# Kernel optimization log

Measured on AMD Instinct MI355X. Metric: run time of the kernel, lower is better.

The kernel has to match this reference:

```python
import jax, jax.numpy as jnp
import numpy as np

N = 50000      # nodes
M = 600000     # message edges (rows of e2)
E = 1600000    # bond-graph edges
H = 128        # hidden_channels
OE = 256       # out_emb_channels
OC = 1         # out_channels
NL = 3         # num_output_layers
ED = 8         # edge_dim


def _glorot(key, shape):
    fan_in = shape[-1]
    return jax.random.normal(key, shape, jnp.float32) / jnp.sqrt(jnp.float32(fan_in))


def setup_inputs() -> dict:
    key = jax.random.key(0)
    ks = jax.random.split(key, 24)
    inp = {}
    inp["e2"] = jax.random.normal(ks[0], (M, H), jnp.float32)
    inp["i"] = jax.random.randint(ks[1], (M,), 0, N)
    inp["afe"] = jax.random.normal(ks[2], (N, 7), jnp.float32)
    inp["b_edge_index"] = jax.random.randint(ks[3], (2, E), 0, N)
    inp["b_edge_attr"] = jax.random.uniform(ks[4], (E, ED), jnp.float32)
    # lin_v: Linear(H+7, H)
    inp["lin_v_w"] = _glorot(ks[5], (H, H + 7))
    inp["lin_v_b"] = jnp.zeros((H,), jnp.float32)
    # PDNConv (shared across both calls): lin (no bias) + edge MLP 8->8->1
    inp["conv_lin_w"] = _glorot(ks[6], (H, H))
    inp["mlp_w1"] = _glorot(ks[7], (ED, ED))
    inp["mlp_b1"] = jnp.zeros((ED,), jnp.float32)
    inp["mlp_w2"] = _glorot(ks[8], (1, ED))
    inp["mlp_b2"] = jnp.zeros((1,), jnp.float32)
    # lin_up: Linear(H, OE)
    inp["lin_up_w"] = _glorot(ks[9], (OE, H))
    inp["lin_up_b"] = jnp.zeros((OE,), jnp.float32)
    # output MLP stack: NL x Linear(OE, OE)
    inp["lins_w"] = _glorot(ks[10], (NL, OE, OE))
    inp["lins_b"] = jnp.zeros((NL, OE), jnp.float32)
    # final lin: Linear(OE, OC, bias=False)
    inp["lin_w"] = _glorot(ks[11], (OC, OE))
    return inp


def reference(e2, i, afe, b_edge_index, b_edge_attr,
              lin_v_w, lin_v_b, conv_lin_w, mlp_w1, mlp_b1, mlp_w2, mlp_b2,
              lin_up_w, lin_up_b, lins_w, lins_b, lin_w):
    # v = scatter_sum(e2, i) over nodes
    v = jax.ops.segment_sum(e2, i, num_segments=N)          # [N, H]
    v = jnp.concatenate([v, afe], axis=1) @ lin_v_w.T + lin_v_b  # [N, H]

    # PDNConv edge weights (shared by both conv calls): mlp(edge_attr) -> sigmoid scalar
    h = jnp.maximum(b_edge_attr @ mlp_w1.T + mlp_b1, 0.0)
    ew = jax.nn.sigmoid(h @ mlp_w2.T + mlp_b2)[:, 0]        # [E]
    row, col = b_edge_index[0], b_edge_index[1]
    # gcn_norm (no self loops): deg over destination, symmetric normalization
    deg = jax.ops.segment_sum(ew, col, num_segments=N)
    dinv = jnp.where(deg > 0, jax.lax.rsqrt(jnp.maximum(deg, 1e-30)), 0.0)
    norm = dinv[row] * ew * dinv[col]                        # [E]

    def conv(x):
        xw = x @ conv_lin_w.T                                # [N, H]
        return jax.ops.segment_sum(xw[row] * norm[:, None], col, num_segments=N)

    v = conv(v)
    v = conv(v)
    v = jax.nn.relu(v)

    v = v @ lin_up_w.T + lin_up_b                            # [N, OE]
    for l in range(NL):
        v = jax.nn.relu(v @ lins_w[l].T + lins_b[l])
    v = v @ lin_w.T                                          # [N, OC]
    return v
```

## Files before the change

### kernel.cpp

```cpp
#include <hip/hip_runtime.h>


#define Nn 50000
#define Mm 600000
#define Ee 1600000
#define NB 196

typedef unsigned short u16;
typedef unsigned int u32;
typedef __attribute__((ext_vector_type(8))) short bh8;
typedef __attribute__((ext_vector_type(4))) float f4;

__device__ __forceinline__ float bf2f(u16 u) {
    union { u32 i; float f; } v; v.i = ((u32)u) << 16; return v.f;
}
__device__ __forceinline__ u16 f2bf(float f) {
    union { float f; u32 u; } v; v.f = f;
    return (u16)((v.u + 0x7fffu + ((v.u >> 16) & 1u)) >> 16);
}

__global__ __launch_bounds__(256) void k_edge(
    const float* __restrict__ attr, const int* __restrict__ eidx,
    const float* __restrict__ w1, const float* __restrict__ b1,
    const float* __restrict__ w2, const float* __restrict__ b2,
    float* __restrict__ ew, float* __restrict__ deg, int* __restrict__ cntC)
{
    __shared__ float sW1[64], sB1[8], sW2[8], sB2;
    int t = threadIdx.x;
    if (t < 64) sW1[t] = w1[t];
    if (t < 8) { sB1[t] = b1[t]; sW2[t] = w2[t]; }
    if (t == 0) sB2 = b2[0];
    __syncthreads();
    int e = blockIdx.x * 256 + t;
    if (e >= Ee) return;
    float4 q0 = *(const float4*)(attr + (size_t)e * 8);
    float4 q1 = *(const float4*)(attr + (size_t)e * 8 + 4);
    float a[8] = { q0.x, q0.y, q0.z, q0.w, q1.x, q1.y, q1.z, q1.w };
    float z = sB2;
#pragma unroll
    for (int j = 0; j < 8; ++j) {
        float h = sB1[j];
#pragma unroll
        for (int k = 0; k < 8; ++k) h += a[k] * sW1[j * 8 + k];
        z += fmaxf(h, 0.f) * sW2[j];
    }
    float s = 1.f / (1.f + __expf(-z));
    ew[e] = s;
    int c = eidx[Ee + e];
    atomicAdd(&deg[c], s);
    atomicAdd(&cntC[c], 1);
}

__global__ __launch_bounds__(256) void k_cntm(const int* __restrict__ ii,
                                              int* __restrict__ cnt)
{
    int m = blockIdx.x * 256 + threadIdx.x;
    if (m < Mm) atomicAdd(&cnt[ii[m]], 1);
}

__global__ __launch_bounds__(256) void k_scanA(
    const int* __restrict__ cnt, int* __restrict__ loc, int* __restrict__ part)
{
    __shared__ int buf[256];
    int t = threadIdx.x, i = blockIdx.x * 256 + t;
    int v = (i < Nn) ? cnt[i] : 0;
    buf[t] = v;
    __syncthreads();
#pragma unroll
    for (int d = 1; d < 256; d <<= 1) {
        int x = (t >= d) ? buf[t - d] : 0;
        __syncthreads();
        buf[t] += x;
        __syncthreads();
    }
    if (i < Nn) loc[i] = buf[t] - v;
    if (t == 255) part[blockIdx.x] = buf[255];
}

__global__ __launch_bounds__(256) void k_scanB(int* __restrict__ pA,
                                               int* __restrict__ pB)
{
    int* p = blockIdx.x ? pB : pA;
    __shared__ int buf[256];
    int t = threadIdx.x;
    int v = (t < NB) ? p[t] : 0;
    buf[t] = v;
    __syncthreads();
#pragma unroll
    for (int d = 1; d < 256; d <<= 1) {
        int x = (t >= d) ? buf[t - d] : 0;
        __syncthreads();
        buf[t] += x;
        __syncthreads();
    }
    if (t < NB) p[t] = buf[t] - v;
}

__global__ __launch_bounds__(256) void k_scanC(
    const int* __restrict__ cnt, const int* __restrict__ part,
    int* __restrict__ off, int* __restrict__ cur,
    const float* __restrict__ deg, float* __restrict__ dinv)
{
    int t = threadIdx.x, i = blockIdx.x * 256 + t;
    if (i >= Nn) return;
    int v = off[i] + part[blockIdx.x];
    off[i] = v;
    cur[i] = v;
    if (i == Nn - 1) off[Nn] = v + cnt[i];
    if (dinv) {
        float d = deg[i];
        dinv[i] = (d > 0.f) ? rsqrtf(fmaxf(d, 1e-30f)) : 0.f;
    }
}

__global__ __launch_bounds__(256) void k_scatter_col(
    const int* __restrict__ eidx, const float* __restrict__ ew,
    const float* __restrict__ dinv, int* __restrict__ cur,
    int2* __restrict__ edgep)
{
    int e = blockIdx.x * 256 + threadIdx.x;
    if (e >= Ee) return;
    int r = eidx[e], c = eidx[Ee + e];
    float nm = dinv[r] * ew[e] * dinv[c];
    int idx = atomicAdd(&cur[c], 1);
    edgep[idx] = make_int2(r, __float_as_int(nm));
}

__global__ __launch_bounds__(256) void k_scatter_m(
    const int* __restrict__ ii, int* __restrict__ cur, int* __restrict__ midx)
{
    int m = blockIdx.x * 256 + threadIdx.x;
    if (m >= Mm) return;
    midx[atomicAdd(&cur[ii[m]], 1)] = m;
}

__global__ __launch_bounds__(256) void k_segsum(
    const int* __restrict__ offM, const int* __restrict__ midx,
    const float* __restrict__ e2, const float* __restrict__ afe,
    float* __restrict__ Xcat)
{
    int wv = threadIdx.x >> 6, lane = threadIdx.x & 63;
    int n = blockIdx.x * 4 + wv;
    if (n >= Nn) return;
    int j0 = offM[n], j1 = offM[n + 1];
    float a0 = 0.f, a1 = 0.f;
    int j = j0;
    if (j < j1) {
        int m = midx[j];
        float2 p = *(const float2*)(e2 + (size_t)m * 128 + lane * 2);
        for (++j; j < j1; ++j) {
            int m2 = midx[j];
            float2 p2 = *(const float2*)(e2 + (size_t)m2 * 128 + lane * 2);
            a0 += p.x; a1 += p.y;
            p = p2;
        }
        a0 += p.x; a1 += p.y;
    }
    *(float2*)(Xcat + (size_t)n * 160 + lane * 2) = make_float2(a0, a1);
    if (lane < 32) {
        int ch = 128 + lane;
        float v = (ch < 135) ? afe[(size_t)n * 7 + (ch - 128)] : 0.f;
        Xcat[(size_t)n * 160 + ch] = v;
    }
}

__global__ __launch_bounds__(256) void k_splitw(
    const float* __restrict__ src, u16* __restrict__ h, u16* __restrict__ l,
    int rows, int sc, int dc)
{
    int idx = blockIdx.x * 256 + threadIdx.x;
    if (idx >= rows * dc) return;
    int r = idx / dc, c = idx % dc;
    float x = (c < sc) ? src[(size_t)r * sc + c] : 0.f;
    u16 hh = f2bf(x);
    h[idx] = hh;
    l[idx] = f2bf(x - bf2f(hh));
}

__global__ __launch_bounds__(256) void k_gemm(
    const float* __restrict__ X, const u16* __restrict__ Wh,
    const u16* __restrict__ Wl, const float* __restrict__ bias,
    void* __restrict__ Y, int M, int K, int NO, int flags)
{
    __shared__ __align__(16) u16 Ah[128][40];
    __shared__ __align__(16) u16 Al[128][40];
    __shared__ __align__(16) u16 Bh[128][40];
    __shared__ __align__(16) u16 Bl[128][40];
    const int t = threadIdx.x;
    const int m0 = blockIdx.x * 128, n0 = blockIdx.y * 128;
    const int lane = t & 63, wv = t >> 6;
    const int wm = (wv >> 1) * 64, wn = (wv & 1) * 64;
    const int lr = lane & 15, lq = lane >> 4;
    const int srow = t >> 1, skc = (t & 1) * 16;
    const bool aok = (m0 + srow) < M;
    const float* Xp = X + (size_t)(m0 + srow) * K + skc;
    const u16* Whp = Wh + (size_t)(n0 + srow) * K + skc;
    const u16* Wlp = Wl + (size_t)(n0 + srow) * K + skc;
    f4 acc[4][4] = {};

    for (int k0 = 0; k0 < K; k0 += 32) {
        float av[16];
#pragma unroll
        for (int g = 0; g < 4; ++g) {
            float4 v = make_float4(0.f, 0.f, 0.f, 0.f);
            if (aok) v = *(const float4*)(Xp + k0 + g * 4);
            av[g * 4 + 0] = v.x; av[g * 4 + 1] = v.y;
            av[g * 4 + 2] = v.z; av[g * 4 + 3] = v.w;
        }
        uint4 bh0 = *(const uint4*)(Whp + k0);
        uint4 bh1 = *(const uint4*)(Whp + k0 + 8);
        uint4 bl0 = *(const uint4*)(Wlp + k0);
        uint4 bl1 = *(const uint4*)(Wlp + k0 + 8);
        __syncthreads();
#pragma unroll
        for (int g = 0; g < 4; ++g) {
            union { u16 s[4]; uint2 d; } h, l;
#pragma unroll
            for (int j = 0; j < 4; ++j) {
                float x = av[g * 4 + j];
                u16 hh = f2bf(x);
                h.s[j] = hh; l.s[j] = f2bf(x - bf2f(hh));
            }
            *(uint2*)&Ah[srow][skc + g * 4] = h.d;
            *(uint2*)&Al[srow][skc + g * 4] = l.d;
        }
        *(uint4*)&Bh[srow][skc]     = bh0;
        *(uint4*)&Bh[srow][skc + 8] = bh1;
        *(uint4*)&Bl[srow][skc]     = bl0;
        *(uint4*)&Bl[srow][skc + 8] = bl1;
        __syncthreads();
        bh8 fah[4], fal[4], fbh[4], fbl[4];
#pragma unroll
        for (int i = 0; i < 4; ++i) {
            fah[i] = *(const bh8*)&Ah[wm + i * 16 + lr][lq * 8];
            fal[i] = *(const bh8*)&Al[wm + i * 16 + lr][lq * 8];
            fbh[i] = *(const bh8*)&Bh[wn + i * 16 + lr][lq * 8];
            fbl[i] = *(const bh8*)&Bl[wn + i * 16 + lr][lq * 8];
        }
#pragma unroll
        for (int mi = 0; mi < 4; ++mi)
#pragma unroll
            for (int ni = 0; ni < 4; ++ni) {
                acc[mi][ni] = __builtin_amdgcn_mfma_f32_16x16x32_bf16(
                    fah[mi], fbh[ni], acc[mi][ni], 0, 0, 0);
                acc[mi][ni] = __builtin_amdgcn_mfma_f32_16x16x32_bf16(
                    fal[mi], fbh[ni], acc[mi][ni], 0, 0, 0);
                acc[mi][ni] = __builtin_amdgcn_mfma_f32_16x16x32_bf16(
                    fah[mi], fbl[ni], acc[mi][ni], 0, 0, 0);
            }
    }
#pragma unroll
    for (int ni = 0; ni < 4; ++ni) {
        int gn = n0 + wn + ni * 16 + lr;
        float bv = bias ? bias[gn] : 0.f;
#pragma unroll
        for (int mi = 0; mi < 4; ++mi) {
#pragma unroll
            for (int r = 0; r < 4; ++r) {
                int gm = m0 + wm + mi * 16 + lq * 4 + r;
                if (gm < M) {
                    float v = acc[mi][ni][r] + bv;
                    if (flags & 1) v = fmaxf(v, 0.f);
                    if (flags & 2) ((u16*)Y)[(size_t)gm * NO + gn] = f2bf(v);
                    else           ((float*)Y)[(size_t)gm * NO + gn] = v;
                }
            }
        }
    }
}

__global__ __launch_bounds__(256) void k_gather(
    const int* __restrict__ off, const int2* __restrict__ edgep,
    const u16* __restrict__ xw, float* __restrict__ out, int relu)
{
    int wv = threadIdx.x >> 6, lane = threadIdx.x & 63;
    int n = blockIdx.x * 4 + wv;
    if (n >= Nn) return;
    int j0 = off[n], j1 = off[n + 1];
    float a0 = 0.f, a1 = 0.f;
    int j = j0;
    if (j < j1) {
        int2 ep = edgep[j];
        u32 p = *(const u32*)(xw + (size_t)ep.x * 128 + lane * 2);
        for (++j; j < j1; ++j) {
            int2 ep2 = edgep[j];
            u32 p2 = *(const u32*)(xw + (size_t)ep2.x * 128 + lane * 2);
            float w = __int_as_float(ep.y);
            a0 += w * bf2f((u16)(p & 0xffff));
            a1 += w * bf2f((u16)(p >> 16));
            ep = ep2; p = p2;
        }
        float w = __int_as_float(ep.y);
        a0 += w * bf2f((u16)(p & 0xffff));
        a1 += w * bf2f((u16)(p >> 16));
    }
    if (relu) { a0 = fmaxf(a0, 0.f); a1 = fmaxf(a1, 0.f); }
    *(float2*)(out + (size_t)n * 128 + lane * 2) = make_float2(a0, a1);
}

__global__ __launch_bounds__(256) void k_final(
    const float* __restrict__ S, const float* __restrict__ lw,
    float* __restrict__ out)
{
    __shared__ float w[256];
    int t = threadIdx.x;
    w[t] = lw[t];
    __syncthreads();
    int n = blockIdx.x * 4 + (t >> 6);
    int lane = t & 63;
    if (n >= Nn) return;
    float s = 0.f;
#pragma unroll
    for (int k = 0; k < 4; ++k)
        s += S[(size_t)n * 256 + lane + k * 64] * w[lane + k * 64];
#pragma unroll
    for (int d = 32; d >= 1; d >>= 1) s += __shfl_xor(s, d, 64);
    if (lane == 0) out[n] = s;
}

extern "C" void kernel_launch(void* const* d_in, const int* in_sizes, int n_in,
                              void* d_out, int out_size, void* d_ws, size_t ws_size,
                              hipStream_t stream)
{
    (void)in_sizes; (void)n_in; (void)out_size; (void)ws_size;
    const float* e2       = (const float*)d_in[0];
    const int*   iidx     = (const int*)d_in[1];
    const float* afe      = (const float*)d_in[2];
    const int*   bei      = (const int*)d_in[3];
    const float* battr    = (const float*)d_in[4];
    const float* lin_v_w  = (const float*)d_in[5];
    const float* lin_v_b  = (const float*)d_in[6];
    const float* conv_w   = (const float*)d_in[7];
    const float* w1       = (const float*)d_in[8];
    const float* b1       = (const float*)d_in[9];
    const float* w2       = (const float*)d_in[10];
    const float* b2       = (const float*)d_in[11];
    const float* lin_up_w = (const float*)d_in[12];
    const float* lin_up_b = (const float*)d_in[13];
    const float* lins_w   = (const float*)d_in[14];
    const float* lins_b   = (const float*)d_in[15];
    const float* lin_w    = (const float*)d_in[16];

    char* ws = (char*)d_ws;
    int2*  edgep = (int2*) (ws + 0);
    float* Xcat  = (float*)(ws + 12800000);
    float* s0    = (float*)(ws + 12800000);
    float* v1    = (float*)(ws + 64000000);
    u16*   xw    = (u16*)  (ws + 89600000);
    float* s1    = (float*)(ws + 64000000);
    float* ew    = (float*)(ws + 102400000);
    int*   midx  = (int*)  (ws + 108800000);
    int*   cntC  = (int*)  (ws + 115200000);
    int*   cntM  = (int*)  (ws + 115400000);
    float* deg   = (float*)(ws + 115600000);
    int*   offC  = (int*)  (ws + 115800000);
    int*   curC  = (int*)  (ws + 116000256);
    int*   offM  = (int*)  (ws + 116200256);
    int*   curM  = (int*)  (ws + 116400512);
    float* dinv  = (float*)(ws + 116600512);
    u16*   Wh    = (u16*)  (ws + 116800512);
    u16*   Wl    = (u16*)  (ws + 117332992);
    int*   partC = (int*)  (ws + 117865472);
    int*   partM = (int*)  (ws + 117866368);

    const int oWv = 0, oConv = 20480, oLup = 36864, oLins = 69632;

    hipMemsetAsync(ws + 115200000, 0, 3 * Nn * 4, stream);

    k_edge<<<(Ee + 255) / 256, 256, 0, stream>>>(battr, bei, w1, b1, w2, b2,
                                                 ew, deg, cntC);
    k_cntm<<<(Mm + 255) / 256, 256, 0, stream>>>(iidx, cntM);
    k_scanA<<<NB, 256, 0, stream>>>(cntC, offC, partC);
    k_scanA<<<NB, 256, 0, stream>>>(cntM, offM, partM);
    k_scanB<<<2, 256, 0, stream>>>(partC, partM);
    k_scanC<<<NB, 256, 0, stream>>>(cntC, partC, offC, curC, deg, dinv);
    k_scanC<<<NB, 256, 0, stream>>>(cntM, partM, offM, curM, nullptr, nullptr);
    k_scatter_col<<<(Ee + 255) / 256, 256, 0, stream>>>(bei, ew, dinv, curC,
                                                        edgep);
    k_scatter_m<<<(Mm + 255) / 256, 256, 0, stream>>>(iidx, curM, midx);
    k_segsum<<<(Nn + 3) / 4, 256, 0, stream>>>(offM, midx, e2, afe, Xcat);

    k_splitw<<<(128 * 160 + 255) / 256, 256, 0, stream>>>(
        lin_v_w, Wh + oWv, Wl + oWv, 128, 135, 160);
    k_splitw<<<(128 * 128 + 255) / 256, 256, 0, stream>>>(
        conv_w, Wh + oConv, Wl + oConv, 128, 128, 128);
    k_splitw<<<(256 * 128 + 255) / 256, 256, 0, stream>>>(
        lin_up_w, Wh + oLup, Wl + oLup, 256, 128, 128);
    k_splitw<<<(768 * 256 + 255) / 256, 256, 0, stream>>>(
        lins_w, Wh + oLins, Wl + oLins, 768, 256, 256);

#define GEMM(Xp, WO, Bp, Yp, M_, K_, NO_, FL_)                                \
    k_gemm<<<dim3(((M_) + 127) / 128, (NO_) / 128), 256, 0, stream>>>(        \
        (const float*)(Xp), Wh + (WO), Wl + (WO), (const float*)(Bp),         \
        (void*)(Yp), M_, K_, NO_, FL_)

    GEMM(Xcat, oWv, lin_v_b, v1, Nn, 160, 128, 0);
    GEMM(v1, oConv, nullptr, xw, Nn, 128, 128, 2);
    k_gather<<<(Nn + 3) / 4, 256, 0, stream>>>(offC, edgep, xw, v1, 0);
    GEMM(v1, oConv, nullptr, xw, Nn, 128, 128, 2);
    k_gather<<<(Nn + 3) / 4, 256, 0, stream>>>(offC, edgep, xw, v1, 1);
    GEMM(v1, oLup, lin_up_b, s0, Nn, 128, 256, 0);
    GEMM(s0, oLins + 0 * 65536, lins_b + 0,   s1, Nn, 256, 256, 1);
    GEMM(s1, oLins + 1 * 65536, lins_b + 256, s0, Nn, 256, 256, 1);
    GEMM(s0, oLins + 2 * 65536, lins_b + 512, s1, Nn, 256, 256, 1);
    k_final<<<(Nn + 3) / 4, 256, 0, stream>>>(s1, lin_w, (float*)d_out);
#undef GEMM
}
```

Measured before the change: 1.235 ms.

## Store activations pre-split as bf16 hi/lo planes and stage GEMM tiles via global_load_lds

Producer kernels (segsum, gather, GEMM epilogue) now write activations as separate bf16 high and low planes instead of fp32. The GEMM no longer converts fp32 to split bf16 on every tile load. Each of the four waves stages one plane directly into LDS with 16-byte global_load_lds, and out-of-range rows are clamped. This removes the per-tile conversion ALU work and register staging. The trade-offs are an unpadded LDS layout that may cause bank conflicts, no prefetch overlap since each load is followed by a barrier, and a larger workspace footprint.

```diff
diff --git a/kernel.cpp b/kernel.cpp
--- a/kernel.cpp
+++ b/kernel.cpp
@@ -18,6 +18,11 @@
     union { float f; u32 u; } v; v.f = f;
     return (u16)((v.u + 0x7fffu + ((v.u >> 16) & 1u)) >> 16);
 }
+
+#define GLD16(gp, lp)                                                         \
+    __builtin_amdgcn_global_load_lds(                                         \
+        (const __attribute__((address_space(1))) unsigned int*)(gp),          \
+        (__attribute__((address_space(3))) unsigned int*)(lp), 16, 0, 0)
 
 __global__ __launch_bounds__(256) void k_edge(
     const float* __restrict__ attr, const int* __restrict__ eidx,
@@ -137,7 +142,7 @@
 __global__ __launch_bounds__(256) void k_segsum(
     const int* __restrict__ offM, const int* __restrict__ midx,
     const float* __restrict__ e2, const float* __restrict__ afe,
-    float* __restrict__ Xcat)
+    u16* __restrict__ XH, u16* __restrict__ XL)
 {
     int wv = threadIdx.x >> 6, lane = threadIdx.x & 63;
     int n = blockIdx.x * 4 + wv;
@@ -156,11 +161,16 @@
         }
         a0 += p.x; a1 += p.y;
     }
-    *(float2*)(Xcat + (size_t)n * 160 + lane * 2) = make_float2(a0, a1);
+    u16 h0 = f2bf(a0), h1 = f2bf(a1);
+    u16 l0 = f2bf(a0 - bf2f(h0)), l1 = f2bf(a1 - bf2f(h1));
+    *(u32*)&XH[(size_t)n * 160 + lane * 2] = (u32)h0 | ((u32)h1 << 16);
+    *(u32*)&XL[(size_t)n * 160 + lane * 2] = (u32)l0 | ((u32)l1 << 16);
     if (lane < 32) {
         int ch = 128 + lane;
         float v = (ch < 135) ? afe[(size_t)n * 7 + (ch - 128)] : 0.f;
-        Xcat[(size_t)n * 160 + ch] = v;
+        u16 h = f2bf(v);
+        XH[(size_t)n * 160 + ch] = h;
+        XL[(size_t)n * 160 + ch] = f2bf(v - bf2f(h));
     }
 }
 
@@ -178,64 +188,42 @@
 }
 
 __global__ __launch_bounds__(256) void k_gemm(
-    const float* __restrict__ X, const u16* __restrict__ Wh,
-    const u16* __restrict__ Wl, const float* __restrict__ bias,
-    void* __restrict__ Y, int M, int K, int NO, int flags)
-{
-    __shared__ __align__(16) u16 Ah[128][40];
-    __shared__ __align__(16) u16 Al[128][40];
-    __shared__ __align__(16) u16 Bh[128][40];
-    __shared__ __align__(16) u16 Bl[128][40];
+    const u16* __restrict__ Ah, const u16* __restrict__ Al,
+    const u16* __restrict__ Bh, const u16* __restrict__ Bl,
+    const float* __restrict__ bias, u16* __restrict__ Yh, u16* __restrict__ Yl,
+    int M, int K, int NO, int flags)
+{
+    __shared__ __align__(16) u16 sT[4][128 * 32];
     const int t = threadIdx.x;
     const int m0 = blockIdx.x * 128, n0 = blockIdx.y * 128;
     const int lane = t & 63, wv = t >> 6;
     const int wm = (wv >> 1) * 64, wn = (wv & 1) * 64;
     const int lr = lane & 15, lq = lane >> 4;
-    const int srow = t >> 1, skc = (t & 1) * 16;
-    const bool aok = (m0 + srow) < M;
-    const float* Xp = X + (size_t)(m0 + srow) * K + skc;
-    const u16* Whp = Wh + (size_t)(n0 + srow) * K + skc;
-    const u16* Wlp = Wl + (size_t)(n0 + srow) * K + skc;
+    const u16* gplane = (wv == 0) ? Ah : (wv == 1) ? Al : (wv == 2) ? Bh : Bl;
+    u16* lplane = &sT[wv][0];
+    const int rbase = (wv < 2) ? m0 : n0;
+    const int rlim = (wv < 2) ? (M - 1) : 0x7fffffff;
+    const int srow = lane >> 2;
+    const int scol = (lane & 3) * 8;
     f4 acc[4][4] = {};
 
     for (int k0 = 0; k0 < K; k0 += 32) {
-        float av[16];
-#pragma unroll
-        for (int g = 0; g < 4; ++g) {
-            float4 v = make_float4(0.f, 0.f, 0.f, 0.f);
-            if (aok) v = *(const float4*)(Xp + k0 + g * 4);
-            av[g * 4 + 0] = v.x; av[g * 4 + 1] = v.y;
-            av[g * 4 + 2] = v.z; av[g * 4 + 3] = v.w;
+        __syncthreads();
+#pragma unroll
+        for (int i = 0; i < 8; ++i) {
+            int grow = rbase + i * 16 + srow;
+            if (grow > rlim) grow = rlim;
+            const u16* gp = gplane + (size_t)grow * K + k0 + scol;
+            GLD16(gp, lplane + i * 512);
         }
-        uint4 bh0 = *(const uint4*)(Whp + k0);
-        uint4 bh1 = *(const uint4*)(Whp + k0 + 8);
-        uint4 bl0 = *(const uint4*)(Wlp + k0);
-        uint4 bl1 = *(const uint4*)(Wlp + k0 + 8);
-        __syncthreads();
-#pragma unroll
-        for (int g = 0; g < 4; ++g) {
-            union { u16 s[4]; uint2 d; } h, l;
-#pragma unroll
-            for (int j = 0; j < 4; ++j) {
-                float x = av[g * 4 + j];
-                u16 hh = f2bf(x);
-                h.s[j] = hh; l.s[j] = f2bf(x - bf2f(hh));
-            }
-            *(uint2*)&Ah[srow][skc + g * 4] = h.d;
-            *(uint2*)&Al[srow][skc + g * 4] = l.d;
-        }
-        *(uint4*)&Bh[srow][skc]     = bh0;
-        *(uint4*)&Bh[srow][skc + 8] = bh1;
-        *(uint4*)&Bl[srow][skc]     = bl0;
-        *(uint4*)&Bl[srow][skc + 8] = bl1;
         __syncthreads();
         bh8 fah[4], fal[4], fbh[4], fbl[4];
 #pragma unroll
         for (int i = 0; i < 4; ++i) {
-            fah[i] = *(const bh8*)&Ah[wm + i * 16 + lr][lq * 8];
-            fal[i] = *(const bh8*)&Al[wm + i * 16 + lr][lq * 8];
-            fbh[i] = *(const bh8*)&Bh[wn + i * 16 + lr][lq * 8];
-            fbl[i] = *(const bh8*)&Bl[wn + i * 16 + lr][lq * 8];
+            fah[i] = *(const bh8*)&sT[0][(wm + i * 16 + lr) * 32 + lq * 8];
+            fal[i] = *(const bh8*)&sT[1][(wm + i * 16 + lr) * 32 + lq * 8];
+            fbh[i] = *(const bh8*)&sT[2][(wn + i * 16 + lr) * 32 + lq * 8];
+            fbl[i] = *(const bh8*)&sT[3][(wn + i * 16 + lr) * 32 + lq * 8];
         }
 #pragma unroll
         for (int mi = 0; mi < 4; ++mi)
@@ -261,8 +249,10 @@
                 if (gm < M) {
                     float v = acc[mi][ni][r] + bv;
                     if (flags & 1) v = fmaxf(v, 0.f);
-                    if (flags & 2) ((u16*)Y)[(size_t)gm * NO + gn] = f2bf(v);
-                    else           ((float*)Y)[(size_t)gm * NO + gn] = v;
+                    u16 h = f2bf(v);
+                    Yh[(size_t)gm * NO + gn] = h;
+                    if (!(flags & 2))
+                        Yl[(size_t)gm * NO + gn] = f2bf(v - bf2f(h));
                 }
             }
         }
@@ -271,7 +261,8 @@
 
 __global__ __launch_bounds__(256) void k_gather(
     const int* __restrict__ off, const int2* __restrict__ edgep,
-    const u16* __restrict__ xw, float* __restrict__ out, int relu)
+    const u16* __restrict__ xw, u16* __restrict__ OH, u16* __restrict__ OL,
+    int relu)
 {
     int wv = threadIdx.x >> 6, lane = threadIdx.x & 63;
     int n = blockIdx.x * 4 + wv;
@@ -295,12 +286,15 @@
         a1 += w * bf2f((u16)(p >> 16));
     }
     if (relu) { a0 = fmaxf(a0, 0.f); a1 = fmaxf(a1, 0.f); }
-    *(float2*)(out + (size_t)n * 128 + lane * 2) = make_float2(a0, a1);
+    u16 h0 = f2bf(a0), h1 = f2bf(a1);
+    u16 l0 = f2bf(a0 - bf2f(h0)), l1 = f2bf(a1 - bf2f(h1));
+    *(u32*)&OH[(size_t)n * 128 + lane * 2] = (u32)h0 | ((u32)h1 << 16);
+    *(u32*)&OL[(size_t)n * 128 + lane * 2] = (u32)l0 | ((u32)l1 << 16);
 }
 
 __global__ __launch_bounds__(256) void k_final(
-    const float* __restrict__ S, const float* __restrict__ lw,
-    float* __restrict__ out)
+    const u16* __restrict__ Sh, const u16* __restrict__ Sl,
+    const float* __restrict__ lw, float* __restrict__ out)
 {
     __shared__ float w[256];
     int t = threadIdx.x;
@@ -311,8 +305,14 @@
     if (n >= Nn) return;
     float s = 0.f;
 #pragma unroll
-    for (int k = 0; k < 4; ++k)
-        s += S[(size_t)n * 256 + lane + k * 64] * w[lane + k * 64];
+    for (int g = 0; g < 2; ++g) {
+        int c = g * 128 + lane * 2;
+        u32 hh = *(const u32*)(Sh + (size_t)n * 256 + c);
+        u32 ll = *(const u32*)(Sl + (size_t)n * 256 + c);
+        float x0 = bf2f((u16)(hh & 0xffff)) + bf2f((u16)(ll & 0xffff));
+        float x1 = bf2f((u16)(hh >> 16)) + bf2f((u16)(ll >> 16));
+        s += x0 * w[c] + x1 * w[c + 1];
+    }
 #pragma unroll
     for (int d = 32; d >= 1; d >>= 1) s += __shfl_xor(s, d, 64);
     if (lane == 0) out[n] = s;
@@ -343,29 +343,35 @@
 
     char* ws = (char*)d_ws;
     int2*  edgep = (int2*) (ws + 0);
-    float* Xcat  = (float*)(ws + 12800000);
-    float* s0    = (float*)(ws + 12800000);
-    float* v1    = (float*)(ws + 64000000);
-    u16*   xw    = (u16*)  (ws + 89600000);
-    float* s1    = (float*)(ws + 64000000);
-    float* ew    = (float*)(ws + 102400000);
-    int*   midx  = (int*)  (ws + 108800000);
-    int*   cntC  = (int*)  (ws + 115200000);
-    int*   cntM  = (int*)  (ws + 115400000);
-    float* deg   = (float*)(ws + 115600000);
-    int*   offC  = (int*)  (ws + 115800000);
-    int*   curC  = (int*)  (ws + 116000256);
-    int*   offM  = (int*)  (ws + 116200256);
-    int*   curM  = (int*)  (ws + 116400512);
-    float* dinv  = (float*)(ws + 116600512);
-    u16*   Wh    = (u16*)  (ws + 116800512);
-    u16*   Wl    = (u16*)  (ws + 117332992);
-    int*   partC = (int*)  (ws + 117865472);
-    int*   partM = (int*)  (ws + 117866368);
+    float* ew    = (float*)(ws + 12800000);
+    int*   midx  = (int*)  (ws + 19200000);
+    int*   cntC  = (int*)  (ws + 21600000);
+    int*   cntM  = (int*)  (ws + 21800000);
+    float* deg   = (float*)(ws + 22000000);
+    int*   offC  = (int*)  (ws + 22200000);
+    int*   curC  = (int*)  (ws + 22400256);
+    int*   offM  = (int*)  (ws + 22600256);
+    int*   curM  = (int*)  (ws + 22800512);
+    float* dinv  = (float*)(ws + 23000512);
+    u16*   Wh    = (u16*)  (ws + 23200512);
+    u16*   Wl    = (u16*)  (ws + 23732992);
+    int*   partC = (int*)  (ws + 24265472);
+    int*   partM = (int*)  (ws + 24266368);
+    u16*   XcatH = (u16*)  (ws + 24268800);
+    u16*   XcatL = (u16*)  (ws + 40268800);
+    u16*   v1h   = (u16*)  (ws + 56268800);
+    u16*   v1l   = (u16*)  (ws + 69068800);
+    u16*   xw    = (u16*)  (ws + 81868800);
+    u16*   gh    = (u16*)  (ws + 94668800);
+    u16*   gl    = (u16*)  (ws + 107468800);
+    u16*   s0h   = (u16*)  (ws + 120268800);
+    u16*   s0l   = (u16*)  (ws + 145868800);
+    u16*   s1h   = (u16*)  (ws + 171468800);
+    u16*   s1l   = (u16*)  (ws + 197068800);
 
     const int oWv = 0, oConv = 20480, oLup = 36864, oLins = 69632;
 
-    hipMemsetAsync(ws + 115200000, 0, 3 * Nn * 4, stream);
+    hipMemsetAsync(ws + 21600000, 0, 3 * Nn * 4, stream);
 
     k_edge<<<(Ee + 255) / 256, 256, 0, stream>>>(battr, bei, w1, b1, w2, b2,
                                                  ew, deg, cntC);
@@ -378,7 +384,8 @@
     k_scatter_col<<<(Ee + 255) / 256, 256, 0, stream>>>(bei, ew, dinv, curC,
                                                         edgep);
     k_scatter_m<<<(Mm + 255) / 256, 256, 0, stream>>>(iidx, curM, midx);
-    k_segsum<<<(Nn + 3) / 4, 256, 0, stream>>>(offM, midx, e2, afe, Xcat);
+    k_segsum<<<(Nn + 3) / 4, 256, 0, stream>>>(offM, midx, e2, afe,
+                                               XcatH, XcatL);
 
     k_splitw<<<(128 * 160 + 255) / 256, 256, 0, stream>>>(
         lin_v_w, Wh + oWv, Wl + oWv, 128, 135, 160);
@@ -389,20 +396,20 @@
     k_splitw<<<(768 * 256 + 255) / 256, 256, 0, stream>>>(
         lins_w, Wh + oLins, Wl + oLins, 768, 256, 256);
 
-#define GEMM(Xp, WO, Bp, Yp, M_, K_, NO_, FL_)                                \
+#define GEMM(XH, XL, WO, Bp, YH, YL, M_, K_, NO_, FL_)                        \
     k_gemm<<<dim3(((M_) + 127) / 128, (NO_) / 128), 256, 0, stream>>>(        \
-        (const float*)(Xp), Wh + (WO), Wl + (WO), (const float*)(Bp),         \
-        (void*)(Yp), M_, K_, NO_, FL_)
-
-    GEMM(Xcat, oWv, lin_v_b, v1, Nn, 160, 128, 0);
-    GEMM(v1, oConv, nullptr, xw, Nn, 128, 128, 2);
-    k_gather<<<(Nn + 3) / 4, 256, 0, stream>>>(offC, edgep, xw, v1, 0);
-    GEMM(v1, oConv, nullptr, xw, Nn, 128, 128, 2);
-    k_gather<<<(Nn + 3) / 4, 256, 0, stream>>>(offC, edgep, xw, v1, 1);
-    GEMM(v1, oLup, lin_up_b, s0, Nn, 128, 256, 0);
-    GEMM(s0, oLins + 0 * 65536, lins_b + 0,   s1, Nn, 256, 256, 1);
-    GEMM(s1, oLins + 1 * 65536, lins_b + 256, s0, Nn, 256, 256, 1);
-    GEMM(s0, oLins + 2 * 65536, lins_b + 512, s1, Nn, 256, 256, 1);
-    k_final<<<(Nn + 3) / 4, 256, 0, stream>>>(s1, lin_w, (float*)d_out);
+        XH, XL, Wh + (WO), Wl + (WO), (const float*)(Bp), YH, YL,             \
+        M_, K_, NO_, FL_)
+
+    GEMM(XcatH, XcatL, oWv, lin_v_b, v1h, v1l, Nn, 160, 128, 0);
+    GEMM(v1h, v1l, oConv, nullptr, xw, nullptr, Nn, 128, 128, 2);
+    k_gather<<<(Nn + 3) / 4, 256, 0, stream>>>(offC, edgep, xw, gh, gl, 0);
+    GEMM(gh, gl, oConv, nullptr, xw, nullptr, Nn, 128, 128, 2);
+    k_gather<<<(Nn + 3) / 4, 256, 0, stream>>>(offC, edgep, xw, gh, gl, 1);
+    GEMM(gh, gl, oLup, lin_up_b, s0h, s0l, Nn, 128, 256, 0);
+    GEMM(s0h, s0l, oLins + 0 * 65536, lins_b + 0,   s1h, s1l, Nn, 256, 256, 1);
+    GEMM(s1h, s1l, oLins + 1 * 65536, lins_b + 256, s0h, s0l, Nn, 256, 256, 1);
+    GEMM(s0h, s0l, oLins + 2 * 65536, lins_b + 512, s1h, s1l, Nn, 256, 256, 1);
+    k_final<<<(Nn + 3) / 4, 256, 0, stream>>>(s1h, s1l, lin_w, (float*)d_out);
 #undef GEMM
 }
```

Result: slower. 1.280 ms (+3.6%).
